# Kernel optimization log

Hardware: AMD Instinct MI355X
Metric: run time of the kernel (lower is better)

## Reference

```python
import jax, jax.numpy as jnp
import numpy as np

TOPK, NC, ALPHA, BETA, EPS = 13, 80, 1.0, 6.0, 1e-9


def _ciou(box1, box2, eps=1e-7):
    # box1, box2: (..., 4) in x1y1x2y2 format; returns CIoU (ultralytics bbox_iou, xywh=False, CIoU=True)
    b1x1, b1y1, b1x2, b1y2 = (box1[..., i] for i in range(4))
    b2x1, b2y1, b2x2, b2y2 = (box2[..., i] for i in range(4))
    w1, h1 = b1x2 - b1x1, b1y2 - b1y1 + eps
    w2, h2 = b2x2 - b2x1, b2y2 - b2y1 + eps
    inter = jnp.clip(jnp.minimum(b1x2, b2x2) - jnp.maximum(b1x1, b2x1), 0.0) * \
            jnp.clip(jnp.minimum(b1y2, b2y2) - jnp.maximum(b1y1, b2y1), 0.0)
    union = w1 * h1 + w2 * h2 - inter + eps
    iou = inter / union
    cw = jnp.maximum(b1x2, b2x2) - jnp.minimum(b1x1, b2x1)  # enclosing box
    ch = jnp.maximum(b1y2, b2y2) - jnp.minimum(b1y1, b2y1)
    c2 = cw ** 2 + ch ** 2 + eps
    rho2 = ((b2x1 + b2x2 - b1x1 - b1x2) ** 2 + (b2y1 + b2y2 - b1y1 - b1y2) ** 2) / 4.0
    v = (4.0 / jnp.pi ** 2) * (jnp.arctan(w2 / h2) - jnp.arctan(w1 / h1)) ** 2
    alpha = jax.lax.stop_gradient(v / (v - iou + (1.0 + eps)))  # torch.no_grad() in original
    return iou - (rho2 / c2 + v * alpha)


def setup_inputs() -> dict:
    key = jax.random.key(0)
    ks = jax.random.split(key, 7)
    B, A, M = 32, 8400, 32
    # multi-level anchor grid over a 640x640 image (strides 8, 16, 32 -> 6400+1600+400=8400)
    pts = []
    for s, n in ((8, 80), (16, 40), (32, 20)):
        xs = (jnp.arange(n, dtype=jnp.float32) + 0.5) * s
        gy, gx = jnp.meshgrid(xs, xs, indexing='ij')
        pts.append(jnp.stack([gx.ravel(), gy.ravel()], -1))
    anc_points = jnp.concatenate(pts, 0)  # (8400, 2)
    pd_scores = jax.random.uniform(ks[0], (B, A, NC), jnp.float32)
    # predicted boxes roughly centered on anchor points
    wh = jax.random.uniform(ks[1], (B, A, 2), jnp.float32, 8.0, 128.0)
    ctr = anc_points[None] + jax.random.normal(ks[2], (B, A, 2), jnp.float32) * 8.0
    pd_bboxes = jnp.concatenate([ctr - wh / 2, ctr + wh / 2], -1)
    gwh = jax.random.uniform(ks[3], (B, M, 2), jnp.float32, 32.0, 256.0)
    gctr = jax.random.uniform(ks[4], (B, M, 2), jnp.float32, 64.0, 576.0)
    gt_bboxes = jnp.concatenate([gctr - gwh / 2, gctr + gwh / 2], -1)
    gt_labels = jax.random.randint(ks[5], (B, M, 1), 0, NC)
    gt_mask = (jax.random.uniform(ks[6], (B, M, 1)) > 0.2).astype(jnp.float32)
    return {"pd_scores": pd_scores, "pd_bboxes": pd_bboxes, "anc_points": anc_points,
            "gt_labels": gt_labels, "gt_bboxes": gt_bboxes, "gt_mask": gt_mask}


def reference(pd_scores, pd_bboxes, anc_points, gt_labels, gt_bboxes, gt_mask):
    B, A, nc = pd_scores.shape
    M = gt_bboxes.shape[1]
    dt = pd_scores.dtype
    gt_mask_f = gt_mask.astype(dt)                              # (B,M,1)

    # --- select_candidates_in_gt: anchors strictly inside each gt box ---
    lt = gt_bboxes[:, :, None, :2]                              # (B,M,1,2)
    rb = gt_bboxes[:, :, None, 2:]
    xy = anc_points[None, None]                                 # (1,1,A,2)
    deltas = jnp.concatenate([xy - lt, rb - xy], -1)            # (B,M,A,4)
    mask_in_gt = (jnp.min(deltas, -1) > EPS).astype(dt)         # (B,M,A)
    fine = (mask_in_gt * gt_mask_f) > 0                         # bool (B,M,A)

    # --- alignment metric: label-indexed score gather + pairwise CIoU ---
    labels = gt_labels[..., 0].astype(jnp.int32)                # (B,M)
    lab_idx = jnp.broadcast_to(labels[:, :, None, None], (B, M, A, 1))
    cls = jnp.take_along_axis(pd_scores[:, None], lab_idx, axis=3)[..., 0]  # (B,M,A)
    pd_scor = jnp.where(fine, cls, 0.0)
    iou = jnp.where(fine, jnp.clip(_ciou(gt_bboxes[:, :, None], pd_bboxes[:, None]), 0.0), 0.0)
    align = pd_scor ** ALPHA * iou ** BETA                      # (B,M,A)

    # --- top-k candidates with duplicate suppression (scatter_add then count>1 -> 0) ---
    _, topk_idx = jax.lax.top_k(align, TOPK)                    # (B,M,K)
    valid = jnp.broadcast_to(gt_mask > 0, (B, M, TOPK))
    topk_idx = jnp.where(valid, topk_idx, 0)
    bi = jnp.arange(B)[:, None, None]
    mi = jnp.arange(M)[None, :, None]
    counts = jnp.zeros((B, M, A), jnp.int32).at[bi, mi, topk_idx].add(1)
    mask_topk = jnp.where(counts > 1, 0, counts).astype(dt)
    mask_pos = gt_mask_f * mask_in_gt * mask_topk               # (B,M,A)

    # --- resolve anchors matched to multiple gts via highest IoU ---
    fg_count = mask_pos.sum(1)                                  # (B,A)
    is_max = jax.nn.one_hot(jnp.argmax(iou, 1), M, dtype=dt).transpose(0, 2, 1)  # (B,M,A)
    mask_pos = jnp.where(fg_count[:, None, :] > 1, is_max, mask_pos)
    fg_mask = mask_pos.sum(1)                                   # (B,A)
    tgt_idx = jnp.argmax(mask_pos, 1)                           # (B,A)

    # --- assign targets ---
    flat_idx = tgt_idx + jnp.arange(B)[:, None] * M             # (B,A)
    target_labels = jnp.clip(labels.reshape(-1)[flat_idx], 0)
    target_bboxes = gt_bboxes.reshape(-1, 4)[flat_idx]          # (B,A,4)
    oh = jax.nn.one_hot(target_labels, NC, dtype=dt)
    target_scores = jnp.where((fg_mask > 0)[..., None], oh, 0.0)

    # --- normalize scores by aligned metric ---
    align = align * mask_pos
    pos_align = jnp.max(align, -1, keepdims=True)               # (B,M,1)
    pos_ov = jnp.max(iou * mask_pos, -1, keepdims=True)         # (B,M,1)
    norm = jnp.max(align * pos_ov / (pos_align + EPS), 1)[..., None]  # (B,A,1)
    target_scores = target_scores * norm

    return target_labels, target_bboxes, target_scores, tgt_idx, fg_mask > 0
```

## Files before the change

kernel.cpp:

```cpp
#include <hip/hip_runtime.h>
#include <cstdint>
#include <cstddef>

constexpr int BB = 32;
constexpr int AA = 8400;
constexpr int MM = 32;
constexpr int CC = 80;
constexpr int KK = 13;
constexpr int CAP = 2048;
constexpr int EMAX = CAP / 256;
constexpr double DEPS = 1e-9;
constexpr double CEPS = 1e-7;
constexpr double PI4 = 0.40528473456935108577;

__device__ __forceinline__ double ciou_f64(
    double gx1, double gy1, double gx2, double gy2,
    double px1, double py1, double px2, double py2)
{
    const double w1 = gx2 - gx1, h1 = gy2 - gy1 + CEPS;
    const double w2 = px2 - px1, h2 = py2 - py1 + CEPS;
    const double iw = fmin(gx2, px2) - fmax(gx1, px1);
    const double ih = fmin(gy2, py2) - fmax(gy1, py1);
    const double inter = fmax(iw, 0.0) * fmax(ih, 0.0);
    const double uni = w1*h1 + w2*h2 - inter + CEPS;
    const double iou = inter / uni;
    const double cw = fmax(gx2, px2) - fmin(gx1, px1);
    const double ch = fmax(gy2, py2) - fmin(gy1, py1);
    const double c2 = cw*cw + ch*ch + CEPS;
    const double ddx = px1 + px2 - gx1 - gx2;
    const double ddy = py1 + py2 - gy1 - gy2;
    const double rho2 = (ddx*ddx + ddy*ddy) * 0.25;
    const double dat = atan(w2 / h2) - atan(w1 / h1);
    const double v = PI4 * (dat * dat);
    const double alpha = v / (v - iou + (1.0 + CEPS));
    return iou - (rho2 / c2 + v * alpha);
}

__global__ __launch_bounds__(256)
void ka_align(const float* __restrict__ pd_scores,
              const float* __restrict__ pd_bboxes,
              const float* __restrict__ anc,
              const int*   __restrict__ gt_labels,
              const float* __restrict__ gt_bboxes,
              const float* __restrict__ gt_mask,
              float* __restrict__ alignf,
              unsigned long long* __restrict__ entries_v,
              int* __restrict__ entries_i,
              int* __restrict__ row_cnt,
              unsigned int* __restrict__ fine_bits)
{
    __shared__ double s_gx1[MM], s_gy1[MM], s_gx2[MM], s_gy2[MM];
    __shared__ double s_w1h1[MM], s_at1[MM];
    __shared__ int s_lab[MM];
    __shared__ unsigned int s_valid;

    const int b = blockIdx.y;
    const int a = blockIdx.x * 256 + threadIdx.x;

    if (threadIdx.x == 0) s_valid = 0;
    __syncthreads();
    if (threadIdx.x < MM) {
        const int m = threadIdx.x;
        const float4 gb = reinterpret_cast<const float4*>(gt_bboxes)[b*MM + m];
        const double gx1 = gb.x, gy1 = gb.y, gx2 = gb.z, gy2 = gb.w;
        s_gx1[m] = gx1; s_gy1[m] = gy1; s_gx2[m] = gx2; s_gy2[m] = gy2;
        const double w1 = gx2 - gx1, h1 = gy2 - gy1 + CEPS;
        s_w1h1[m] = w1 * h1;
        s_at1[m]  = atan(w1 / h1);
        s_lab[m]  = gt_labels[b*MM + m];
        if (gt_mask[b*MM + m] > 0.0f) atomicOr(&s_valid, 1u << m);
    }
    __syncthreads();
    if (a >= AA) return;

    const float2 ap = reinterpret_cast<const float2*>(anc)[a];
    const double ax = ap.x, ay = ap.y;
    const float4 pb = reinterpret_cast<const float4*>(pd_bboxes)[(size_t)b*AA + a];
    const double px1 = pb.x, py1 = pb.y, px2 = pb.z, py2 = pb.w;
    const double w2 = px2 - px1, h2 = py2 - py1 + CEPS;
    const double at2 = atan(w2 / h2);
    const double w2h2 = w2 * h2;
    const float* srow = pd_scores + ((size_t)b*AA + a) * CC;
    const unsigned int vmask = s_valid;
    const size_t obase = (size_t)b * MM * AA + a;
    unsigned int fb = 0;

    #pragma unroll 4
    for (int m = 0; m < MM; ++m) {
        const double gx1 = s_gx1[m], gy1 = s_gy1[m];
        const double gx2 = s_gx2[m], gy2 = s_gy2[m];
        const double mind = fmin(fmin(ax - gx1, ay - gy1),
                                 fmin(gx2 - ax, gy2 - ay));
        const bool fine = (mind > DEPS) && ((vmask >> m) & 1u);

        const double iw = fmin(gx2, px2) - fmax(gx1, px1);
        const double ih = fmin(gy2, py2) - fmax(gy1, py1);
        const double inter = fmax(iw, 0.0) * fmax(ih, 0.0);
        const double uni = s_w1h1[m] + w2h2 - inter + CEPS;
        const double iou = inter / uni;
        const double cw = fmax(gx2, px2) - fmin(gx1, px1);
        const double ch = fmax(gy2, py2) - fmin(gy1, py1);
        const double c2 = cw*cw + ch*ch + CEPS;
        const double ddx = px1 + px2 - gx1 - gx2;
        const double ddy = py1 + py2 - gy1 - gy2;
        const double rho2 = (ddx*ddx + ddy*ddy) * 0.25;
        const double dat = at2 - s_at1[m];
        const double v = PI4 * (dat * dat);
        const double alpha = v / (v - iou + (1.0 + CEPS));
        const double ciou = iou - (rho2 / c2 + v * alpha);

        const double iouc = fine ? fmax(ciou, 0.0) : 0.0;
        const double cls  = fine ? (double)srow[s_lab[m]] : 0.0;
        const double i2 = iouc * iouc;
        const double algn = cls * (i2 * i2 * i2);
        alignf[obase + (size_t)m * AA] = (float)algn;
        if (fine) fb |= 1u << m;
        if (algn > 0.0) {
            const int row = b * MM + m;
            const int slot = atomicAdd(&row_cnt[row], 1);
            if (slot < CAP) {
                entries_v[(size_t)row * CAP + slot] = __double_as_longlong(algn);
                entries_i[(size_t)row * CAP + slot] = a;
            }
        }
    }
    fine_bits[(size_t)b*AA + a] = fb;
}

__global__ __launch_bounds__(256)
void kt_select(const unsigned long long* __restrict__ entries_v,
               const int* __restrict__ entries_i,
               const int* __restrict__ row_cnt,
               const unsigned int* __restrict__ fine_bits,
               const float* __restrict__ gt_mask,
               unsigned int* __restrict__ bits)
{
    __shared__ unsigned long long s_wv[4];
    __shared__ int s_wi[4];
    __shared__ unsigned long long s_gv;
    __shared__ int s_gi;

    const int bm = blockIdx.x;
    if (gt_mask[bm] <= 0.0f) return;
    const int b = bm / MM, m = bm % MM;
    const int c = min(row_cnt[bm], CAP);
    const int tid = threadIdx.x;

    unsigned long long ev[EMAX]; int ei[EMAX];
    #pragma unroll
    for (int s = 0; s < EMAX; ++s) {
        const int e = tid + s * 256;
        const bool ok = e < c;
        ev[s] = ok ? entries_v[(size_t)bm * CAP + e] : 0ull;
        ei[s] = ok ? entries_i[(size_t)bm * CAP + e] : 0x7fffffff;
    }

    unsigned int cons = 0;
    const int rounds = min(c, KK);
    for (int k = 0; k < rounds; ++k) {
        unsigned long long bv = 0ull; int bi = 0x7fffffff;
        #pragma unroll
        for (int s = 0; s < EMAX; ++s) {
            const bool live = !((cons >> s) & 1u);
            if (live && (ev[s] > bv || (ev[s] == bv && ei[s] < bi))) {
                bv = ev[s]; bi = ei[s];
            }
        }
        #pragma unroll
        for (int off = 32; off > 0; off >>= 1) {
            const unsigned long long ov = __shfl_down(bv, off);
            const int oi = __shfl_down(bi, off);
            if (ov > bv || (ov == bv && oi < bi)) { bv = ov; bi = oi; }
        }
        if ((tid & 63) == 0) { s_wv[tid >> 6] = bv; s_wi[tid >> 6] = bi; }
        __syncthreads();
        if (tid == 0) {
            unsigned long long gv = s_wv[0]; int gi = s_wi[0];
            for (int w = 1; w < 4; ++w)
                if (s_wv[w] > gv || (s_wv[w] == gv && s_wi[w] < gi)) {
                    gv = s_wv[w]; gi = s_wi[w];
                }
            s_gv = gv; s_gi = gi;
        }
        __syncthreads();
        const unsigned long long gv = s_gv; const int gi = s_gi;
        #pragma unroll
        for (int s = 0; s < EMAX; ++s) {
            if (!((cons >> s) & 1u) && ei[s] == gi && ev[s] == gv) {
                cons |= 1u << s;
                if (fine_bits[b*AA + gi] & (1u << m))
                    atomicOr(&bits[b*AA + gi], 1u << m);
            }
        }
    }

    if (c < KK && tid == 0) {
        int need = KK - c;
        const int* __restrict__ ip = entries_i + (size_t)bm * CAP;
        for (int a = 0; a < AA && need > 0; ++a) {
            bool inlist = false;
            for (int j = 0; j < c; ++j) if (ip[j] == a) { inlist = true; break; }
            if (!inlist) {
                --need;
                if (fine_bits[b*AA + a] & (1u << m))
                    atomicOr(&bits[b*AA + a], 1u << m);
            }
        }
    }
}

__global__ __launch_bounds__(256)
void kb_resolve(const int*   __restrict__ gt_labels,
                const float* __restrict__ gt_bboxes,
                const float* __restrict__ pd_bboxes,
                const unsigned int* __restrict__ fine_bits,
                const float* __restrict__ alignf,
                unsigned int* __restrict__ bits,
                float* __restrict__ out_labels,
                float* __restrict__ out_bboxes,
                float* __restrict__ out_tgt,
                float* __restrict__ out_fg,
                unsigned int* __restrict__ posal_u,
                unsigned int* __restrict__ posov_u)
{
    const int idx = blockIdx.x * 256 + threadIdx.x;
    if (idx >= BB * AA) return;
    const int b = idx / AA, a = idx - b * AA;

    unsigned int bt = bits[idx];
    const int cnt = __popc(bt);
    int tgt = 0; float fg = 0.0f;

    if (cnt > 0) {
        fg = 1.0f;
        const float4 pb = reinterpret_cast<const float4*>(pd_bboxes)[(size_t)b*AA + a];
        const unsigned int fb = fine_bits[idx];
        double iou_t = 0.0;
        if (cnt > 1) {
            double bestv = -1.0; int bmx = 0;
            for (int m = 0; m < MM; ++m) {
                double v = 0.0;
                if ((fb >> m) & 1u) {
                    const float4 gb = reinterpret_cast<const float4*>(gt_bboxes)[b*MM + m];
                    v = fmax(ciou_f64(gb.x, gb.y, gb.z, gb.w, pb.x, pb.y, pb.z, pb.w), 0.0);
                }
                if (v > bestv) { bestv = v; bmx = m; }
            }
            tgt = bmx; bt = 1u << bmx; iou_t = bestv;
        } else {
            tgt = __ffs(bt) - 1;
            if ((fb >> tgt) & 1u) {
                const float4 gb = reinterpret_cast<const float4*>(gt_bboxes)[b*MM + tgt];
                iou_t = fmax(ciou_f64(gb.x, gb.y, gb.z, gb.w, pb.x, pb.y, pb.z, pb.w), 0.0);
            }
        }
        const float al = alignf[((size_t)b*MM + tgt)*AA + a];
        atomicMax(&posal_u[b*MM + tgt], __float_as_uint(al));
        atomicMax(&posov_u[b*MM + tgt], __float_as_uint((float)iou_t));
    }
    bits[idx] = bt;

    int lab = gt_labels[b*MM + tgt];
    if (lab < 0) lab = 0;
    out_labels[idx] = (float)lab;
    reinterpret_cast<float4*>(out_bboxes)[idx] =
        reinterpret_cast<const float4*>(gt_bboxes)[b*MM + tgt];
    out_tgt[idx] = (float)tgt;
    out_fg[idx]  = fg;
}

__global__ __launch_bounds__(256)
void kd1_norm(const unsigned int* __restrict__ bits,
              const float* __restrict__ alignf,
              const unsigned int* __restrict__ posal_u,
              const unsigned int* __restrict__ posov_u,
              float* __restrict__ ws_norm)
{
    const int idx = blockIdx.x * 256 + threadIdx.x;
    if (idx >= BB * AA) return;
    const int b = idx / AA, a = idx - b * AA;
    const unsigned int bt = bits[idx];
    double nv = 0.0;
    if (bt) {
        const int m = __ffs(bt) - 1;
        nv = (double)alignf[((size_t)b*MM + m)*AA + a]
           * (double)__uint_as_float(posov_u[b*MM + m])
           / ((double)__uint_as_float(posal_u[b*MM + m]) + DEPS);
    }
    ws_norm[idx] = (float)nv;
}

__global__ __launch_bounds__(256)
void kd2_scores(const float* __restrict__ out_labels,
                const float* __restrict__ out_fg,
                const float* __restrict__ ws_norm,
                float* __restrict__ out_scores)
{
    const int i = blockIdx.x * 256 + threadIdx.x;
    if (i >= BB * AA * (CC/4)) return;
    const int cell = i / (CC/4);
    const int q = (i - cell * (CC/4)) * 4;
    float4 r = make_float4(0.f, 0.f, 0.f, 0.f);
    if (out_fg[cell] > 0.0f) {
        const int lab = (int)out_labels[cell];
        if (lab >= q && lab < q + 4) {
            const float n = ws_norm[cell];
            if (lab == q)     r.x = n;
            if (lab == q + 1) r.y = n;
            if (lab == q + 2) r.z = n;
            if (lab == q + 3) r.w = n;
        }
    }
    reinterpret_cast<float4*>(out_scores)[i] = r;
}

extern "C" void kernel_launch(void* const* d_in, const int* in_sizes, int n_in,
                              void* d_out, int out_size, void* d_ws, size_t ws_size,
                              hipStream_t stream)
{
    const float* pd_scores = (const float*)d_in[0];
    const float* pd_bboxes = (const float*)d_in[1];
    const float* anc       = (const float*)d_in[2];
    const int*   gt_labels = (const int*)d_in[3];
    const float* gt_bboxes = (const float*)d_in[4];
    const float* gt_mask   = (const float*)d_in[5];

    char* ws = (char*)d_ws;
    unsigned long long* entries_v = (unsigned long long*)ws;
    ws += (size_t)BB*MM*CAP*8;
    float* alignf = (float*)ws;              ws += (size_t)BB*MM*AA*4;
    int* entries_i = (int*)ws;               ws += (size_t)BB*MM*CAP*4;
    unsigned int* fine_bits = (unsigned int*)ws; ws += (size_t)BB*AA*4;
    unsigned int* bits = (unsigned int*)ws;      ws += (size_t)BB*AA*4;
    unsigned int* posal_u = (unsigned int*)ws;   ws += (size_t)BB*MM*4;
    unsigned int* posov_u = (unsigned int*)ws;   ws += (size_t)BB*MM*4;
    int* row_cnt = (int*)ws;                     ws += (size_t)BB*MM*4;
    float* ws_norm = (float*)ws;                 ws += (size_t)BB*AA*4;

    float* out = (float*)d_out;
    float* out_labels = out;
    float* out_bboxes = out + (size_t)BB*AA;
    float* out_scores = out + (size_t)BB*AA*5;
    float* out_tgt    = out + (size_t)BB*AA*(5+CC);
    float* out_fg     = out + (size_t)BB*AA*(6+CC);

    hipMemsetAsync(bits, 0, (size_t)BB*AA*4 + (size_t)BB*MM*12, stream);

    dim3 ga((AA + 255)/256, BB);
    ka_align<<<ga, 256, 0, stream>>>(pd_scores, pd_bboxes, anc, gt_labels,
                                     gt_bboxes, gt_mask, alignf,
                                     entries_v, entries_i, row_cnt, fine_bits);
    kt_select<<<BB*MM, 256, 0, stream>>>(entries_v, entries_i, row_cnt,
                                         fine_bits, gt_mask, bits);
    kb_resolve<<<(BB*AA + 255)/256, 256, 0, stream>>>(gt_labels, gt_bboxes, pd_bboxes,
                                                      fine_bits, alignf, bits,
                                                      out_labels, out_bboxes,
                                                      out_tgt, out_fg,
                                                      posal_u, posov_u);
    kd1_norm<<<(BB*AA + 255)/256, 256, 0, stream>>>(bits, alignf, posal_u,
                                                    posov_u, ws_norm);
    kd2_scores<<<(BB*AA*(CC/4) + 255)/256, 256, 0, stream>>>(out_labels, out_fg,
                                                             ws_norm, out_scores);
}
```

Measured before the change: 98.66 us.

## Drop dense align matrix; recompute align for assigned target and fuse norm kernel

```diff
diff --git a/kernel.cpp b/kernel.cpp
--- a/kernel.cpp
+++ b/kernel.cpp
@@ -43,7 +43,6 @@
               const int*   __restrict__ gt_labels,
               const float* __restrict__ gt_bboxes,
               const float* __restrict__ gt_mask,
-              float* __restrict__ alignf,
               unsigned long long* __restrict__ entries_v,
               int* __restrict__ entries_i,
               int* __restrict__ row_cnt,
@@ -82,7 +81,6 @@
     const double w2h2 = w2 * h2;
     const float* srow = pd_scores + ((size_t)b*AA + a) * CC;
     const unsigned int vmask = s_valid;
-    const size_t obase = (size_t)b * MM * AA + a;
     unsigned int fb = 0;
 
     #pragma unroll 4
@@ -92,6 +90,7 @@
         const double mind = fmin(fmin(ax - gx1, ay - gy1),
                                  fmin(gx2 - ax, gy2 - ay));
         const bool fine = (mind > DEPS) && ((vmask >> m) & 1u);
+        if (!fine) continue;
 
         const double iw = fmin(gx2, px2) - fmax(gx1, px1);
         const double ih = fmin(gy2, py2) - fmax(gy1, py1);
@@ -109,12 +108,11 @@
         const double alpha = v / (v - iou + (1.0 + CEPS));
         const double ciou = iou - (rho2 / c2 + v * alpha);
 
-        const double iouc = fine ? fmax(ciou, 0.0) : 0.0;
-        const double cls  = fine ? (double)srow[s_lab[m]] : 0.0;
+        const double iouc = fmax(ciou, 0.0);
+        const double cls  = (double)srow[s_lab[m]];
         const double i2 = iouc * iouc;
         const double algn = cls * (i2 * i2 * i2);
-        alignf[obase + (size_t)m * AA] = (float)algn;
-        if (fine) fb |= 1u << m;
+        fb |= 1u << m;
         if (algn > 0.0) {
             const int row = b * MM + m;
             const int slot = atomicAdd(&row_cnt[row], 1);
@@ -213,13 +211,14 @@
 void kb_resolve(const int*   __restrict__ gt_labels,
                 const float* __restrict__ gt_bboxes,
                 const float* __restrict__ pd_bboxes,
+                const float* __restrict__ pd_scores,
                 const unsigned int* __restrict__ fine_bits,
-                const float* __restrict__ alignf,
                 unsigned int* __restrict__ bits,
                 float* __restrict__ out_labels,
                 float* __restrict__ out_bboxes,
                 float* __restrict__ out_tgt,
                 float* __restrict__ out_fg,
+                float* __restrict__ ws_alout,
                 unsigned int* __restrict__ posal_u,
                 unsigned int* __restrict__ posov_u)
 {
@@ -229,7 +228,7 @@
 
     unsigned int bt = bits[idx];
     const int cnt = __popc(bt);
-    int tgt = 0; float fg = 0.0f;
+    int tgt = 0; float fg = 0.0f; float alout = 0.0f;
 
     if (cnt > 0) {
         fg = 1.0f;
@@ -249,13 +248,14 @@
             tgt = bmx; bt = 1u << bmx; iou_t = bestv;
         } else {
             tgt = __ffs(bt) - 1;
-            if ((fb >> tgt) & 1u) {
-                const float4 gb = reinterpret_cast<const float4*>(gt_bboxes)[b*MM + tgt];
-                iou_t = fmax(ciou_f64(gb.x, gb.y, gb.z, gb.w, pb.x, pb.y, pb.z, pb.w), 0.0);
-            }
-        }
-        const float al = alignf[((size_t)b*MM + tgt)*AA + a];
-        atomicMax(&posal_u[b*MM + tgt], __float_as_uint(al));
+            const float4 gb = reinterpret_cast<const float4*>(gt_bboxes)[b*MM + tgt];
+            iou_t = fmax(ciou_f64(gb.x, gb.y, gb.z, gb.w, pb.x, pb.y, pb.z, pb.w), 0.0);
+        }
+        const double cls = (double)pd_scores[((size_t)b*AA + a) * CC
+                                             + max(gt_labels[b*MM + tgt], 0)];
+        const double i2 = iou_t * iou_t;
+        alout = (float)(cls * (i2 * i2 * i2));
+        atomicMax(&posal_u[b*MM + tgt], __float_as_uint(alout));
         atomicMax(&posov_u[b*MM + tgt], __float_as_uint((float)iou_t));
     }
     bits[idx] = bt;
@@ -267,33 +267,16 @@
         reinterpret_cast<const float4*>(gt_bboxes)[b*MM + tgt];
     out_tgt[idx] = (float)tgt;
     out_fg[idx]  = fg;
-}
-
-__global__ __launch_bounds__(256)
-void kd1_norm(const unsigned int* __restrict__ bits,
-              const float* __restrict__ alignf,
-              const unsigned int* __restrict__ posal_u,
-              const unsigned int* __restrict__ posov_u,
-              float* __restrict__ ws_norm)
-{
-    const int idx = blockIdx.x * 256 + threadIdx.x;
-    if (idx >= BB * AA) return;
-    const int b = idx / AA, a = idx - b * AA;
-    const unsigned int bt = bits[idx];
-    double nv = 0.0;
-    if (bt) {
-        const int m = __ffs(bt) - 1;
-        nv = (double)alignf[((size_t)b*MM + m)*AA + a]
-           * (double)__uint_as_float(posov_u[b*MM + m])
-           / ((double)__uint_as_float(posal_u[b*MM + m]) + DEPS);
-    }
-    ws_norm[idx] = (float)nv;
+    ws_alout[idx] = alout;
 }
 
 __global__ __launch_bounds__(256)
 void kd2_scores(const float* __restrict__ out_labels,
                 const float* __restrict__ out_fg,
-                const float* __restrict__ ws_norm,
+                const float* __restrict__ out_tgt,
+                const float* __restrict__ ws_alout,
+                const unsigned int* __restrict__ posal_u,
+                const unsigned int* __restrict__ posov_u,
                 float* __restrict__ out_scores)
 {
     const int i = blockIdx.x * 256 + threadIdx.x;
@@ -304,7 +287,12 @@
     if (out_fg[cell] > 0.0f) {
         const int lab = (int)out_labels[cell];
         if (lab >= q && lab < q + 4) {
-            const float n = ws_norm[cell];
+            const int b = cell / AA;
+            const int m = (int)out_tgt[cell];
+            const double nv = (double)ws_alout[cell]
+                            * (double)__uint_as_float(posov_u[b*MM + m])
+                            / ((double)__uint_as_float(posal_u[b*MM + m]) + DEPS);
+            const float n = (float)nv;
             if (lab == q)     r.x = n;
             if (lab == q + 1) r.y = n;
             if (lab == q + 2) r.z = n;
@@ -328,14 +316,13 @@
     char* ws = (char*)d_ws;
     unsigned long long* entries_v = (unsigned long long*)ws;
     ws += (size_t)BB*MM*CAP*8;
-    float* alignf = (float*)ws;              ws += (size_t)BB*MM*AA*4;
     int* entries_i = (int*)ws;               ws += (size_t)BB*MM*CAP*4;
     unsigned int* fine_bits = (unsigned int*)ws; ws += (size_t)BB*AA*4;
     unsigned int* bits = (unsigned int*)ws;      ws += (size_t)BB*AA*4;
     unsigned int* posal_u = (unsigned int*)ws;   ws += (size_t)BB*MM*4;
     unsigned int* posov_u = (unsigned int*)ws;   ws += (size_t)BB*MM*4;
     int* row_cnt = (int*)ws;                     ws += (size_t)BB*MM*4;
-    float* ws_norm = (float*)ws;                 ws += (size_t)BB*AA*4;
+    float* ws_alout = (float*)ws;                ws += (size_t)BB*AA*4;
 
     float* out = (float*)d_out;
     float* out_labels = out;
@@ -348,17 +335,17 @@
 
     dim3 ga((AA + 255)/256, BB);
     ka_align<<<ga, 256, 0, stream>>>(pd_scores, pd_bboxes, anc, gt_labels,
-                                     gt_bboxes, gt_mask, alignf,
+                                     gt_bboxes, gt_mask,
                                      entries_v, entries_i, row_cnt, fine_bits);
     kt_select<<<BB*MM, 256, 0, stream>>>(entries_v, entries_i, row_cnt,
                                          fine_bits, gt_mask, bits);
     kb_resolve<<<(BB*AA + 255)/256, 256, 0, stream>>>(gt_labels, gt_bboxes, pd_bboxes,
-                                                      fine_bits, alignf, bits,
+                                                      pd_scores, fine_bits, bits,
                                                       out_labels, out_bboxes,
-                                                      out_tgt, out_fg,
+                                                      out_tgt, out_fg, ws_alout,
                                                       posal_u, posov_u);
-    kd1_norm<<<(BB*AA + 255)/256, 256, 0, stream>>>(bits, alignf, posal_u,
-                                                    posov_u, ws_norm);
     kd2_scores<<<(BB*AA*(CC/4) + 255)/256, 256, 0, stream>>>(out_labels, out_fg,
-                                                             ws_norm, out_scores);
-}
+                                                             out_tgt, ws_alout,
+                                                             posal_u, posov_u,
+                                                             out_scores);
+}
```

Result: faster. 96.41 us (-2.3%).
